# Kernel optimization log

Measured on AMD Instinct MI355X. Metric: run time of the kernel, lower is better.

## Reference

```python
import jax, jax.numpy as jnp
import numpy as np

EPS = 1e-7  # keras backend.epsilon()
KSZ = 3
STRIDE = 1
NUM_CAPS = 32        # output capsule types
NUM_CAPS_IN = 32     # input capsule types
POSE = 4             # 4x4 pose matrices
ROUTINGS = 3


def _patches(t, k, s):
    # t: [B, H, W, C] -> [B, Ho, Wo, k*k, C], patch index order i*k+j (row-major),
    # matching the tf depthwise_conv2d tile-filter trick + transpose in the source.
    B, H, W, C = t.shape
    Ho = (H - k) // s + 1
    Wo = (W - k) // s + 1
    return jnp.stack(
        [t[:, i:i + Ho * s:s, j:j + Wo * s:s, :] for i in range(k) for j in range(k)],
        axis=3,
    )


def setup_inputs() -> dict:
    key = jax.random.key(0)
    k1, k2, k3, k4 = jax.random.split(key, 4)
    B, H, W = 2, 14, 14
    KKI = KSZ * KSZ * NUM_CAPS_IN  # 288
    x = jax.random.normal(k1, (B, H, W, NUM_CAPS_IN, POSE * POSE + 1), dtype=jnp.float32)
    Wt = jax.random.normal(k2, (KKI, NUM_CAPS, POSE, POSE), dtype=jnp.float32) * 0.05
    beta_v = jax.random.normal(k3, (1, 1, 1, 1, NUM_CAPS, 1), dtype=jnp.float32) * 0.1
    beta_a = jax.random.normal(k4, (1, 1, 1, 1, NUM_CAPS, 1), dtype=jnp.float32) * 0.1
    return {"x": x, "W": Wt, "beta_v": beta_v, "beta_a": beta_a}


def _em_routing(V, a_i, beta_v, beta_a):
    # V: [B,Ho,Wo,KKI,NC,PP], a_i: [B,Ho,Wo,KKI,1,1]
    KKI, NC = V.shape[3], V.shape[4]
    R = jnp.full((KKI, NC, 1), 1.0 / NC, dtype=V.dtype)
    M_j = a_j = None
    for it in range(ROUTINGS):
        inv_temp = 1.0 + (min(ROUTINGS, 3.0) - 1.0) * it / max(1.0, ROUTINGS - 1.0)
        # --- maximization ---
        Rw = R * a_i                                    # [B,Ho,Wo,KKI,NC,1]
        Rsum = jnp.sum(Rw, axis=-3, keepdims=True)      # [B,Ho,Wo,1,NC,1]
        M_jk = jnp.sum(Rw * V, axis=-3, keepdims=True) / Rsum   # [B,Ho,Wo,1,NC,PP]
        # NOTE: source uses R_ij_sum (not R_ij) inside the variance sum; keep faithful.
        stdv = jnp.sqrt(jnp.sum(Rsum * jnp.square(V - M_jk), axis=-3, keepdims=True) / Rsum)
        cost_h = (beta_v + jnp.log(stdv + EPS)) * Rsum
        cost = jnp.sum(cost_h, axis=-1, keepdims=True)          # [B,Ho,Wo,1,NC,1]
        c_mean = jnp.mean(cost, axis=-2, keepdims=True)
        c_stdv = jnp.sqrt(jnp.sum(jnp.square(cost - c_mean), axis=-2, keepdims=True) / NC)
        a_cost = beta_a + (c_mean - cost) / (c_stdv + EPS)
        a_jk = jax.nn.sigmoid(inv_temp * a_cost)                # [B,Ho,Wo,1,NC,1]
        a_j = jnp.squeeze(jnp.squeeze(a_jk, axis=-3), axis=-1)  # [B,Ho,Wo,NC]
        M_j = jnp.squeeze(M_jk, axis=-3)                        # [B,Ho,Wo,NC,PP]
        if it < ROUTINGS - 1:
            # --- estimation ---
            log_a = jnp.log(a_j[..., None, :, None] + EPS)      # [B,Ho,Wo,1,NC,1]
            log_p = (log_a
                     - jnp.sum(jnp.square(V - M_jk) / (2.0 * jnp.square(stdv)), axis=-1, keepdims=True)
                     - jnp.sum(jnp.log(stdv + EPS), axis=-1, keepdims=True))
            R = jax.nn.softmax(log_p, axis=-2)                  # softmax over NC axis
    return M_j, a_j


def reference(x, W, beta_v, beta_a):
    B, H, Wd, Cin, _ = x.shape
    PP = POSE * POSE
    M_i = x[..., :PP]          # [B,H,W,Cin,16]
    a_i = x[..., PP]           # [B,H,W,Cin]
    # depthwise-conv patch extraction (conv path)
    Mp = _patches(M_i.reshape(B, H, Wd, Cin * PP), KSZ, STRIDE)   # [B,Ho,Wo,9,Cin*16]
    B_, Ho, Wo = Mp.shape[0], Mp.shape[1], Mp.shape[2]
    KKI = KSZ * KSZ * Cin
    Mp = Mp.reshape(B, Ho, Wo, KKI, POSE, POSE)
    ap = _patches(a_i, KSZ, STRIDE).reshape(B, Ho, Wo, KKI)
    # spatial transform: vote matrices V_ij = M_i @ W_ij
    V = jnp.einsum('bhwipq,icqr->bhwicpr', Mp, W)                 # [B,Ho,Wo,KKI,NC,4,4]
    V = V.reshape(B, Ho, Wo, KKI, NUM_CAPS, PP)
    a_in = ap[..., None, None]                                    # [B,Ho,Wo,KKI,1,1]
    M_j, a_j = _em_routing(V, a_in, beta_v, beta_a)
    # assemble output: [B,Ho,Wo,NC,16] poses concat sigmoid activation
    out = jnp.concatenate([M_j, jax.nn.sigmoid(a_j)[..., None]], axis=-1)
    return out  # [B,Ho,Wo,NC,17]
```

## Files before the change

kernel.cpp:

```cpp
#include <hip/hip_runtime.h>
#include <math.h>


#define EPSF 1e-7f
#define KKI 288
#define NC 32
#define NTHREADS 512
#define IPT 18
#define ST 17
#define L2E 1.4426950408889634f

__device__ __forceinline__ float rcp_fast(float v) { return __builtin_amdgcn_rcpf(v); }

template <int CTRL>
__device__ __forceinline__ float dpp_mov_f(float x) {
    return __int_as_float(__builtin_amdgcn_update_dpp(
        0, __float_as_int(x), CTRL, 0xF, 0xF, true));
}
__device__ __forceinline__ float row_sum16(float x) {
    x += dpp_mov_f<0xB1>(x);
    x += dpp_mov_f<0x4E>(x);
    x += dpp_mov_f<0x124>(x);
    x += dpp_mov_f<0x128>(x);
    return x;
}
__device__ __forceinline__ float row_max16(float x) {
    x = fmaxf(x, dpp_mov_f<0xB1>(x));
    x = fmaxf(x, dpp_mov_f<0x4E>(x));
    x = fmaxf(x, dpp_mov_f<0x124>(x));
    x = fmaxf(x, dpp_mov_f<0x128>(x));
    return x;
}

__global__ __launch_bounds__(NTHREADS)
void caps_em_kernel(const float* __restrict__ x, const float* __restrict__ Wg,
                    const float* __restrict__ beta_v, const float* __restrict__ beta_a,
                    float* __restrict__ out)
{
    __shared__ float MpL[KKI * 16];
    __shared__ float apL[KKI];
    __shared__ float T1L[NC * ST];
    __shared__ float S1L[NC * ST];
    __shared__ float S2L[NC * ST];
    __shared__ float ML[NC * ST];
    __shared__ float I2L[NC * ST];
    __shared__ float RsumL[NC];
    __shared__ float constL[NC];
    __shared__ float slogL[NC];
    __shared__ float costL[NC];
    __shared__ float aoutL[NC];
    __shared__ float KmaxL;

    const int t = threadIdx.x;
    const int bid = blockIdx.x;
    const int b = bid / 144;
    const int rem = bid - b * 144;
    const int ho = rem / 12;
    const int wo = rem - ho * 12;

    const int c = t & 31;
    const int isub = t >> 5;
    const int iBase = isub * IPT;

    for (int idx = t; idx < KKI * 17; idx += NTHREADS) {
        int i = idx / 17;
        int e = idx - i * 17;
        int p = i >> 5, cin = i & 31;
        int di = p / 3, dj = p - di * 3;
        float vx = x[(((b * 14 + (ho + di)) * 14 + (wo + dj)) * 32 + cin) * 17 + e];
        if (e < 16) MpL[i * 16 + e] = vx; else apL[i] = vx;
    }
    for (int idx = t; idx < NC * ST; idx += NTHREADS) { T1L[idx] = 0.f; S1L[idx] = 0.f; S2L[idx] = 0.f; }
    if (t < NC) RsumL[t] = 0.f;
    __syncthreads();

    auto statsA = [&]() {
        const int cc = t >> 4, d = t & 15;
        float rsum = RsumL[cc];
        float m = T1L[cc * ST + d] * rcp_fast(rsum);
        float var = S2L[cc * ST + d] - 2.f * m * S1L[cc * ST + d] + 288.f * m * m;
        var = fmaxf(var, 0.f);
        float lg = logf(sqrtf(var) + EPSF);
        ML[cc * ST + d] = m;
        I2L[cc * ST + d] = 0.5f * rcp_fast(var);
        float sl = row_sum16(lg);
        if (d == 0) {
            slogL[cc] = sl;
            costL[cc] = rsum * (16.f * beta_v[cc] + sl);
        }
    };
    auto statsB = [&](float inv_temp) {
        if (t < 32) {
            float cost = costL[t];
            float csum = row_sum16(cost); csum += __shfl_xor(csum, 16);
            float c_mean = csum * 0.03125f;
            float diff = cost - c_mean;
            float dsq = row_sum16(diff * diff); dsq += __shfl_xor(dsq, 16);
            float c_stdv = sqrtf(dsq * 0.03125f);
            float a_cost = beta_a[t] + (c_mean - cost) * rcp_fast(c_stdv + EPSF);
            float a_j = 1.f / (1.f + expf(-inv_temp * a_cost));
            float kc = logf(a_j + EPSF) - slogL[t];
            constL[t] = kc;
            aoutL[t] = 1.f / (1.f + expf(-a_j));
            float km = row_max16(kc); km = fmaxf(km, __shfl_xor(km, 16));
            if (t == 0) KmaxL = km;
        }
    };

    {
        float t1[16], s1[16], s2[16];
        #pragma unroll
        for (int d = 0; d < 16; ++d) { t1[d] = 0.f; s1[d] = 0.f; s2[d] = 0.f; }
        float rsum = 0.f;
        for (int j = 0; j < IPT; ++j) {
            const int i = iBase + j;
            float wa[16], ma[16];
            const float4* w4 = (const float4*)(Wg + ((size_t)((i << 5) + c) << 4));
            ((float4*)wa)[0] = w4[0]; ((float4*)wa)[1] = w4[1];
            ((float4*)wa)[2] = w4[2]; ((float4*)wa)[3] = w4[3];
            const float4* mp4 = (const float4*)(MpL + (i << 4));
            ((float4*)ma)[0] = mp4[0]; ((float4*)ma)[1] = mp4[1];
            ((float4*)ma)[2] = mp4[2]; ((float4*)ma)[3] = mp4[3];
            float rw = apL[i] * 0.03125f;
            rsum += rw;
            #pragma unroll
            for (int p = 0; p < 4; ++p)
                #pragma unroll
                for (int r = 0; r < 4; ++r) {
                    float acc = ma[p * 4 + 0] * wa[0 * 4 + r];
                    acc = fmaf(ma[p * 4 + 1], wa[1 * 4 + r], acc);
                    acc = fmaf(ma[p * 4 + 2], wa[2 * 4 + r], acc);
                    acc = fmaf(ma[p * 4 + 3], wa[3 * 4 + r], acc);
                    const int d = p * 4 + r;
                    t1[d] = fmaf(rw, acc, t1[d]);
                    s1[d] += acc;
                    s2[d] = fmaf(acc, acc, s2[d]);
                }
        }
        rsum += __shfl_xor(rsum, 32);
        #pragma unroll
        for (int d = 0; d < 16; ++d) {
            t1[d] += __shfl_xor(t1[d], 32);
            s1[d] += __shfl_xor(s1[d], 32);
            s2[d] += __shfl_xor(s2[d], 32);
        }
        if ((t & 32) == 0) {
            atomicAdd(&RsumL[c], rsum);
            #pragma unroll
            for (int d = 0; d < 16; ++d) {
                atomicAdd(&T1L[c * ST + d], t1[d]);
                atomicAdd(&S1L[c * ST + d], s1[d]);
                atomicAdd(&S2L[c * ST + d], s2[d]);
            }
        }
        __syncthreads();
        statsA();
        __syncthreads();
        statsB(1.0f);
        __syncthreads();
    }

    for (int it = 1; it < 3; ++it) {
        float Mreg[16], i2[16];
        #pragma unroll
        for (int d = 0; d < 16; ++d) {
            Mreg[d] = ML[c * ST + d];
            i2[d]   = I2L[c * ST + d] * L2E;
        }
        float Kc2 = (constL[c] - KmaxL) * L2E;
        __syncthreads();
        for (int idx = t; idx < NC * ST; idx += NTHREADS) T1L[idx] = 0.f;
        if (t < NC) RsumL[t] = 0.f;
        __syncthreads();

        float t1[16];
        #pragma unroll
        for (int d = 0; d < 16; ++d) t1[d] = 0.f;
        float rsum = 0.f;
        for (int j = 0; j < IPT; ++j) {
            const int i = iBase + j;
            float wa[16], ma[16];
            const float4* w4 = (const float4*)(Wg + ((size_t)((i << 5) + c) << 4));
            ((float4*)wa)[0] = w4[0]; ((float4*)wa)[1] = w4[1];
            ((float4*)wa)[2] = w4[2]; ((float4*)wa)[3] = w4[3];
            const float4* mp4 = (const float4*)(MpL + (i << 4));
            ((float4*)ma)[0] = mp4[0]; ((float4*)ma)[1] = mp4[1];
            ((float4*)ma)[2] = mp4[2]; ((float4*)ma)[3] = mp4[3];
            float a_i = apL[i];
            float v[16];
            #pragma unroll
            for (int p = 0; p < 4; ++p)
                #pragma unroll
                for (int r = 0; r < 4; ++r) {
                    float acc = ma[p * 4 + 0] * wa[0 * 4 + r];
                    acc = fmaf(ma[p * 4 + 1], wa[1 * 4 + r], acc);
                    acc = fmaf(ma[p * 4 + 2], wa[2 * 4 + r], acc);
                    acc = fmaf(ma[p * 4 + 3], wa[3 * 4 + r], acc);
                    v[p * 4 + r] = acc;
                }
            float lp2 = Kc2;
            #pragma unroll
            for (int d = 0; d < 16; ++d) {
                float df = v[d] - Mreg[d];
                lp2 = fmaf(-df * df, i2[d], lp2);
            }
            float ex = exp2f(lp2);
            float ssum = row_sum16(ex);
            ssum += __shfl_xor(ssum, 16);
            float rw = ex * rcp_fast(ssum) * a_i;
            rsum += rw;
            #pragma unroll
            for (int d = 0; d < 16; ++d) t1[d] = fmaf(rw, v[d], t1[d]);
        }
        rsum += __shfl_xor(rsum, 32);
        #pragma unroll
        for (int d = 0; d < 16; ++d) t1[d] += __shfl_xor(t1[d], 32);
        if ((t & 32) == 0) {
            atomicAdd(&RsumL[c], rsum);
            #pragma unroll
            for (int d = 0; d < 16; ++d) atomicAdd(&T1L[c * ST + d], t1[d]);
        }
        __syncthreads();
        statsA();
        __syncthreads();
        statsB(1.0f + (float)it);
        __syncthreads();
    }

    for (int idx = t; idx < NC * 17; idx += NTHREADS) {
        int cc = idx / 17;
        int e = idx - cc * 17;
        float val = (e < 16) ? ML[idx] : aoutL[cc];
        out[(size_t)bid * (NC * 17) + idx] = val;
    }
}

extern "C" void kernel_launch(void* const* d_in, const int* in_sizes, int n_in,
                              void* d_out, int out_size, void* d_ws, size_t ws_size,
                              hipStream_t stream) {
    const float* x  = (const float*)d_in[0];
    const float* W  = (const float*)d_in[1];
    const float* bv = (const float*)d_in[2];
    const float* ba = (const float*)d_in[3];
    float* out = (float*)d_out;
    caps_em_kernel<<<288, NTHREADS, 0, stream>>>(x, W, bv, ba, out);
}
```

Measured before the change: 180.4 us.

## Pack two output positions per 1024-thread block and split log-prob accumulation

Each block now handles two spatial positions with 1024 threads (two independent 512-thread halves with separate shared buffers), launching 144 blocks instead of 288. The log2e scaling is folded into the stored inverse variance, and the 16-term log-probability reduction is split into two independent accumulators to shorten the dependency chain. The block merge leaves half the CUs unused on a chip with more than 144 CUs, and the halves now share barriers. In exchange it may improve latency hiding per CU.

Measured after the change: 169.8 us. 5.9% less time.

```diff
diff --git a/kernel.cpp b/kernel.cpp
--- a/kernel.cpp
+++ b/kernel.cpp
@@ -5,7 +5,8 @@
 #define EPSF 1e-7f
 #define KKI 288
 #define NC 32
-#define NTHREADS 512
+#define NTHREADS 1024
+#define UNIT 512
 #define IPT 18
 #define ST 17
 #define L2E 1.4426950408889634f
@@ -37,73 +38,75 @@
                     const float* __restrict__ beta_v, const float* __restrict__ beta_a,
                     float* __restrict__ out)
 {
-    __shared__ float MpL[KKI * 16];
-    __shared__ float apL[KKI];
-    __shared__ float T1L[NC * ST];
-    __shared__ float S1L[NC * ST];
-    __shared__ float S2L[NC * ST];
-    __shared__ float ML[NC * ST];
-    __shared__ float I2L[NC * ST];
-    __shared__ float RsumL[NC];
-    __shared__ float constL[NC];
-    __shared__ float slogL[NC];
-    __shared__ float costL[NC];
-    __shared__ float aoutL[NC];
-    __shared__ float KmaxL;
+    __shared__ float MpL[2][KKI * 16];
+    __shared__ float apL[2][KKI];
+    __shared__ float T1L[2][NC * ST];
+    __shared__ float S1L[2][NC * ST];
+    __shared__ float S2L[2][NC * ST];
+    __shared__ float ML[2][NC * ST];
+    __shared__ float I2L[2][NC * ST];
+    __shared__ float RsumL[2][NC];
+    __shared__ float constL[2][NC];
+    __shared__ float slogL[2][NC];
+    __shared__ float costL[2][NC];
+    __shared__ float aoutL[2][NC];
+    __shared__ float KmaxL[2];
 
     const int t = threadIdx.x;
-    const int bid = blockIdx.x;
-    const int b = bid / 144;
-    const int rem = bid - b * 144;
+    const int H = t >> 9;
+    const int u = t & 511;
+    const int pos = blockIdx.x * 2 + H;
+    const int b = pos / 144;
+    const int rem = pos - b * 144;
     const int ho = rem / 12;
     const int wo = rem - ho * 12;
 
-    const int c = t & 31;
-    const int isub = t >> 5;
+    const int c = u & 31;
+    const int isub = u >> 5;
     const int iBase = isub * IPT;
 
-    for (int idx = t; idx < KKI * 17; idx += NTHREADS) {
+    for (int idx = u; idx < KKI * 17; idx += UNIT) {
         int i = idx / 17;
         int e = idx - i * 17;
         int p = i >> 5, cin = i & 31;
         int di = p / 3, dj = p - di * 3;
         float vx = x[(((b * 14 + (ho + di)) * 14 + (wo + dj)) * 32 + cin) * 17 + e];
-        if (e < 16) MpL[i * 16 + e] = vx; else apL[i] = vx;
-    }
-    for (int idx = t; idx < NC * ST; idx += NTHREADS) { T1L[idx] = 0.f; S1L[idx] = 0.f; S2L[idx] = 0.f; }
-    if (t < NC) RsumL[t] = 0.f;
+        if (e < 16) MpL[H][i * 16 + e] = vx; else apL[H][i] = vx;
+    }
+    for (int idx = u; idx < NC * ST; idx += UNIT) { T1L[H][idx] = 0.f; S1L[H][idx] = 0.f; S2L[H][idx] = 0.f; }
+    if (u < NC) RsumL[H][u] = 0.f;
     __syncthreads();
 
     auto statsA = [&]() {
-        const int cc = t >> 4, d = t & 15;
-        float rsum = RsumL[cc];
-        float m = T1L[cc * ST + d] * rcp_fast(rsum);
-        float var = S2L[cc * ST + d] - 2.f * m * S1L[cc * ST + d] + 288.f * m * m;
+        const int cc = u >> 4, d = u & 15;
+        float rsum = RsumL[H][cc];
+        float m = T1L[H][cc * ST + d] * rcp_fast(rsum);
+        float var = S2L[H][cc * ST + d] - 2.f * m * S1L[H][cc * ST + d] + 288.f * m * m;
         var = fmaxf(var, 0.f);
         float lg = logf(sqrtf(var) + EPSF);
-        ML[cc * ST + d] = m;
-        I2L[cc * ST + d] = 0.5f * rcp_fast(var);
+        ML[H][cc * ST + d] = m;
+        I2L[H][cc * ST + d] = 0.5f * L2E * rcp_fast(var);
         float sl = row_sum16(lg);
         if (d == 0) {
-            slogL[cc] = sl;
-            costL[cc] = rsum * (16.f * beta_v[cc] + sl);
+            slogL[H][cc] = sl;
+            costL[H][cc] = rsum * (16.f * beta_v[cc] + sl);
         }
     };
     auto statsB = [&](float inv_temp) {
-        if (t < 32) {
-            float cost = costL[t];
+        if (u < 32) {
+            float cost = costL[H][u];
             float csum = row_sum16(cost); csum += __shfl_xor(csum, 16);
             float c_mean = csum * 0.03125f;
             float diff = cost - c_mean;
             float dsq = row_sum16(diff * diff); dsq += __shfl_xor(dsq, 16);
             float c_stdv = sqrtf(dsq * 0.03125f);
-            float a_cost = beta_a[t] + (c_mean - cost) * rcp_fast(c_stdv + EPSF);
+            float a_cost = beta_a[u] + (c_mean - cost) * rcp_fast(c_stdv + EPSF);
             float a_j = 1.f / (1.f + expf(-inv_temp * a_cost));
-            float kc = logf(a_j + EPSF) - slogL[t];
-            constL[t] = kc;
-            aoutL[t] = 1.f / (1.f + expf(-a_j));
+            float kc = logf(a_j + EPSF) - slogL[H][u];
+            constL[H][u] = kc;
+            aoutL[H][u] = 1.f / (1.f + expf(-a_j));
             float km = row_max16(kc); km = fmaxf(km, __shfl_xor(km, 16));
-            if (t == 0) KmaxL = km;
+            if (u == 0) KmaxL[H] = km;
         }
     };
 
@@ -118,10 +121,10 @@
             const float4* w4 = (const float4*)(Wg + ((size_t)((i << 5) + c) << 4));
             ((float4*)wa)[0] = w4[0]; ((float4*)wa)[1] = w4[1];
             ((float4*)wa)[2] = w4[2]; ((float4*)wa)[3] = w4[3];
-            const float4* mp4 = (const float4*)(MpL + (i << 4));
+            const float4* mp4 = (const float4*)(&MpL[H][i << 4]);
             ((float4*)ma)[0] = mp4[0]; ((float4*)ma)[1] = mp4[1];
             ((float4*)ma)[2] = mp4[2]; ((float4*)ma)[3] = mp4[3];
-            float rw = apL[i] * 0.03125f;
+            float rw = apL[H][i] * 0.03125f;
             rsum += rw;
             #pragma unroll
             for (int p = 0; p < 4; ++p)
@@ -144,13 +147,13 @@
             s1[d] += __shfl_xor(s1[d], 32);
             s2[d] += __shfl_xor(s2[d], 32);
         }
-        if ((t & 32) == 0) {
-            atomicAdd(&RsumL[c], rsum);
+        if ((u & 32) == 0) {
+            atomicAdd(&RsumL[H][c], rsum);
             #pragma unroll
             for (int d = 0; d < 16; ++d) {
-                atomicAdd(&T1L[c * ST + d], t1[d]);
-                atomicAdd(&S1L[c * ST + d], s1[d]);
-                atomicAdd(&S2L[c * ST + d], s2[d]);
+                atomicAdd(&T1L[H][c * ST + d], t1[d]);
+                atomicAdd(&S1L[H][c * ST + d], s1[d]);
+                atomicAdd(&S2L[H][c * ST + d], s2[d]);
             }
         }
         __syncthreads();
@@ -164,13 +167,13 @@
         float Mreg[16], i2[16];
         #pragma unroll
         for (int d = 0; d < 16; ++d) {
-            Mreg[d] = ML[c * ST + d];
-            i2[d]   = I2L[c * ST + d] * L2E;
-        }
-        float Kc2 = (constL[c] - KmaxL) * L2E;
-        __syncthreads();
-        for (int idx = t; idx < NC * ST; idx += NTHREADS) T1L[idx] = 0.f;
-        if (t < NC) RsumL[t] = 0.f;
+            Mreg[d] = ML[H][c * ST + d];
+            i2[d]   = I2L[H][c * ST + d];
+        }
+        float Kc2 = (constL[H][c] - KmaxL[H]) * L2E;
+        __syncthreads();
+        for (int idx = u; idx < NC * ST; idx += UNIT) T1L[H][idx] = 0.f;
+        if (u < NC) RsumL[H][u] = 0.f;
         __syncthreads();
 
         float t1[16];
@@ -183,10 +186,10 @@
             const float4* w4 = (const float4*)(Wg + ((size_t)((i << 5) + c) << 4));
             ((float4*)wa)[0] = w4[0]; ((float4*)wa)[1] = w4[1];
             ((float4*)wa)[2] = w4[2]; ((float4*)wa)[3] = w4[3];
-            const float4* mp4 = (const float4*)(MpL + (i << 4));
+            const float4* mp4 = (const float4*)(&MpL[H][i << 4]);
             ((float4*)ma)[0] = mp4[0]; ((float4*)ma)[1] = mp4[1];
             ((float4*)ma)[2] = mp4[2]; ((float4*)ma)[3] = mp4[3];
-            float a_i = apL[i];
+            float a_i = apL[H][i];
             float v[16];
             #pragma unroll
             for (int p = 0; p < 4; ++p)
@@ -198,13 +201,18 @@
                     acc = fmaf(ma[p * 4 + 3], wa[3 * 4 + r], acc);
                     v[p * 4 + r] = acc;
                 }
-            float lp2 = Kc2;
-            #pragma unroll
-            for (int d = 0; d < 16; ++d) {
+            float lpa = 0.f, lpb = 0.f;
+            #pragma unroll
+            for (int d = 0; d < 8; ++d) {
                 float df = v[d] - Mreg[d];
-                lp2 = fmaf(-df * df, i2[d], lp2);
+                lpa = fmaf(-df * df, i2[d], lpa);
             }
-            float ex = exp2f(lp2);
+            #pragma unroll
+            for (int d = 8; d < 16; ++d) {
+                float df = v[d] - Mreg[d];
+                lpb = fmaf(-df * df, i2[d], lpb);
+            }
+            float ex = exp2f(Kc2 + lpa + lpb);
             float ssum = row_sum16(ex);
             ssum += __shfl_xor(ssum, 16);
             float rw = ex * rcp_fast(ssum) * a_i;
@@ -215,10 +223,10 @@
         rsum += __shfl_xor(rsum, 32);
         #pragma unroll
         for (int d = 0; d < 16; ++d) t1[d] += __shfl_xor(t1[d], 32);
-        if ((t & 32) == 0) {
-            atomicAdd(&RsumL[c], rsum);
-            #pragma unroll
-            for (int d = 0; d < 16; ++d) atomicAdd(&T1L[c * ST + d], t1[d]);
+        if ((u & 32) == 0) {
+            atomicAdd(&RsumL[H][c], rsum);
+            #pragma unroll
+            for (int d = 0; d < 16; ++d) atomicAdd(&T1L[H][c * ST + d], t1[d]);
         }
         __syncthreads();
         statsA();
@@ -227,11 +235,11 @@
         __syncthreads();
     }
 
-    for (int idx = t; idx < NC * 17; idx += NTHREADS) {
+    for (int idx = u; idx < NC * 17; idx += UNIT) {
         int cc = idx / 17;
         int e = idx - cc * 17;
-        float val = (e < 16) ? ML[idx] : aoutL[cc];
-        out[(size_t)bid * (NC * 17) + idx] = val;
+        float val = (e < 16) ? ML[H][idx] : aoutL[H][cc];
+        out[(size_t)pos * (NC * 17) + idx] = val;
     }
 }
 
@@ -243,5 +251,5 @@
     const float* bv = (const float*)d_in[2];
     const float* ba = (const float*)d_in[3];
     float* out = (float*)d_out;
-    caps_em_kernel<<<288, NTHREADS, 0, stream>>>(x, W, bv, ba, out);
-}
+    caps_em_kernel<<<144, NTHREADS, 0, stream>>>(x, W, bv, ba, out);
+}
```
